# Performance work log

Hardware: AMD Instinct MI355X
Metric: run time of the kernel (lower is better)

The kernel has to match this reference:

```python
import jax, jax.numpy as jnp
import numpy as np

F = 50  # number of feature fields

def setup_inputs() -> dict:
    key = jax.random.key(0)
    k1, k2, k3, k4 = jax.random.split(key, 4)
    B, D, A = 4096, 16, 32
    return {
        "feat_emb": jax.random.normal(k1, (B, F, D), dtype=jnp.float32),
        "W": jax.random.normal(k2, (D, A), dtype=jnp.float32) * 0.1,
        "h": jax.random.normal(k3, (A,), dtype=jnp.float32),
        "p_vec": jax.random.normal(k4, (D,), dtype=jnp.float32),
    }

def reference(feat_emb, W, h, p_vec):
    # build_cross: upper-triangular field pairs (i < j)
    row, col = np.triu_indices(F, k=1)              # each [P], P = F*(F-1)/2
    p = feat_emb[:, row]                             # [B, P, D]
    q = feat_emb[:, col]                             # [B, P, D]
    inter = p * q                                    # pairwise interaction [B, P, D]
    # AttLayer: Dense(no bias) -> relu -> contract with h -> softmax over pairs
    att_signal = jax.nn.relu(jnp.einsum('bpd,da->bpa', inter, W))  # [B, P, A]
    scores = jnp.einsum('bpa,a->bp', att_signal, h)                # [B, P]
    att = jax.nn.softmax(scores, axis=1)                           # [B, P]
    # attention-weighted sum-pooling over pairs
    pooled = jnp.einsum('bp,bpd->bd', att, inter)                  # [B, D]
    # dropout omitted (inference); final projection and reduce
    out = jnp.einsum('bd,d->b', pooled, p_vec)[:, None]            # [B, 1]
    return out
```

## Files before the change

### kernel.cpp

```cpp
#include <hip/hip_runtime.h>
#include <math.h>


#define FF 50
#define DD 16
#define AA 32
#define NP 1225
#define NT 39
#define NTP 40
#define ERS 24
#define EBS (FF * ERS)
#define BPB 8
#define NTHR 512
#define SGN (NT * 32)

typedef _Float16 half8 __attribute__((ext_vector_type(8)));
typedef _Float16 half4 __attribute__((ext_vector_type(4)));
typedef _Float16 half2v __attribute__((ext_vector_type(2)));
typedef __fp16   fh2    __attribute__((ext_vector_type(2)));
typedef float    floatx16 __attribute__((ext_vector_type(16)));

__global__ __launch_bounds__(NTHR, 2) void afm_kernel(
    const float* __restrict__ feat,
    const float* __restrict__ W,
    const float* __restrict__ h,
    const float* __restrict__ pvec,
    float* __restrict__ out,
    int Btot)
{
  __shared__ __align__(16) _Float16 eh[BPB * EBS];
  __shared__ unsigned int tbl[NTP * 32];
  __shared__ __align__(16) float2 sg[BPB * SGN];

  const int tid    = threadIdx.x;
  const int lane   = tid & 63;
  const int wave   = tid >> 6;
  const int halfid = lane >> 5;
  const int n      = lane & 31;
  const int b0     = blockIdx.x * BPB;

  for (int s = tid; s < BPB * 200; s += NTHR) {
    int bl  = s / 200;
    int rem = s - bl * 200;
    int bb  = b0 + bl;
    if (bb < Btot) {
      float4 v4 = ((const float4*)feat)[(size_t)bb * 200 + rem];
      half4 hv;
      hv[0] = (_Float16)v4.x; hv[1] = (_Float16)v4.y;
      hv[2] = (_Float16)v4.z; hv[3] = (_Float16)v4.w;
      int row = rem >> 2, q = rem & 3;
      *(half4*)(&eh[bl * EBS + row * ERS + q * 4]) = hv;
    }
  }

  for (int q = tid; q < NTP * 32; q += NTHR) {
    int t = ((q >> 6) << 1) | (q & 1);
    int nn = (q >> 1) & 31;
    int p = t * 32 + nn;
    unsigned ent = 0;
    if (p < NP) {
      int rad = 9801 - 8 * p;
      int i = (int)((99.0f - sqrtf((float)rad)) * 0.5f);
      if (i < 0) i = 0; if (i > 48) i = 48;
      int off = (i * (99 - i)) >> 1;
      if (off > p) { --i; off = (i * (99 - i)) >> 1; }
      else {
        int off1 = ((i + 1) * (98 - i)) >> 1;
        if (off1 <= p) { ++i; off = off1; }
      }
      int j = p - off + i + 1;
      ent = ((unsigned)(i * 48) << 16) | (unsigned)(j * 48);
    }
    tbl[q] = ent;
  }

  const float LOG2E = 1.4426950408889634f;
  half8 A0;
  #pragma unroll
  for (int jj = 0; jj < 8; ++jj)
    A0[jj] = (_Float16)W[(halfid * 8 + jj) * AA + n];
  float hreg[16];
  #pragma unroll
  for (int r = 0; r < 16; ++r)
    hreg[r] = h[(r & 3) + 8 * (r >> 2) + 4 * halfid] * LOG2E;
  fh2 pv2[4];
  #pragma unroll
  for (int q = 0; q < 4; ++q) {
    pv2[q][0] = (__fp16)pvec[halfid * 8 + 2 * q];
    pv2[q][1] = (__fp16)pvec[halfid * 8 + 2 * q + 1];
  }
  const floatx16 ZACC = (floatx16)0.0f;

  __syncthreads();

  const char* eb = (const char*)(eh + wave * EBS) + halfid * 16;
  float2* sgw = sg + wave * SGN;
  const unsigned int* tpair = tbl + 2 * n;

  auto core = [&](unsigned oi, unsigned oj, float& vout, float& gout) {
    half8 Bi = *(const half8*)(eb + oi);
    half8 Bj = *(const half8*)(eb + oj);
    half8 Bv = Bi * Bj;
    floatx16 z = __builtin_amdgcn_mfma_f32_32x32x16_f16(A0, Bv, ZACC, 0, 0, 0);
    float a0 = 0.f, a1 = 0.f, a2 = 0.f, a3 = 0.f;
    #pragma unroll
    for (int r = 0; r < 16; r += 4) {
      a0 = fmaf(fmaxf(z[r + 0], 0.f), hreg[r + 0], a0);
      a1 = fmaf(fmaxf(z[r + 1], 0.f), hreg[r + 1], a1);
      a2 = fmaf(fmaxf(z[r + 2], 0.f), hreg[r + 2], a2);
      a3 = fmaf(fmaxf(z[r + 3], 0.f), hreg[r + 3], a3);
    }
    float v = (a0 + a1) + (a2 + a3);
#if __has_builtin(__builtin_amdgcn_fdot2)
    fh2 q0 = __builtin_bit_cast(fh2, (half2v)__builtin_shufflevector(Bv, Bv, 0, 1));
    fh2 q1 = __builtin_bit_cast(fh2, (half2v)__builtin_shufflevector(Bv, Bv, 2, 3));
    fh2 q2 = __builtin_bit_cast(fh2, (half2v)__builtin_shufflevector(Bv, Bv, 4, 5));
    fh2 q3 = __builtin_bit_cast(fh2, (half2v)__builtin_shufflevector(Bv, Bv, 6, 7));
    float g = __builtin_amdgcn_fdot2(q1, pv2[1],
              __builtin_amdgcn_fdot2(q0, pv2[0], 0.f, false), false)
            + __builtin_amdgcn_fdot2(q3, pv2[3],
              __builtin_amdgcn_fdot2(q2, pv2[2], 0.f, false), false);
#else
    float g = 0.f;
    #pragma unroll
    for (int k = 0; k < 8; ++k)
      g = fmaf((float)Bv[k], (float)((const __fp16*)pv2)[k], g);
#endif
    vout = v + __shfl_xor(v, 32, 64);
    gout = g + __shfl_xor(g, 32, 64);
  };

  for (int th = 0; th < 19; ++th) {
    uint2 ij2 = *(const uint2*)(tpair + th * 64);
    float v0, g0, v1, g1;
    core(ij2.x >> 16, ij2.x & 0xffffu, v0, g0);
    core(ij2.y >> 16, ij2.y & 0xffffu, v1, g1);
    if (lane < 32) {
      sgw[(2 * th)     * 32 + n] = make_float2(v0, g0);
      sgw[(2 * th + 1) * 32 + n] = make_float2(v1, g1);
    }
  }
  {
    unsigned ij = tpair[19 * 64];
    float v, g;
    core(ij >> 16, ij & 0xffffu, v, g);
    if (n >= 9) v = -3.0e38f;
    if (lane < 32) sgw[38 * 32 + n] = make_float2(v, g);
  }

  float den = 0.f, num = 0.f;
  for (int p = lane; p < SGN; p += 64) {
    float2 s2 = sgw[p];
    float e = exp2f(s2.x);
    den += e;
    num = fmaf(e, s2.y, num);
  }
  #pragma unroll
  for (int mask = 32; mask >= 1; mask >>= 1) {
    den += __shfl_xor(den, mask, 64);
    num += __shfl_xor(num, mask, 64);
  }
  const int b = b0 + wave;
  if (lane == 0 && b < Btot) out[b] = num / den;
}

extern "C" void kernel_launch(void* const* d_in, const int* in_sizes, int n_in,
                              void* d_out, int out_size, void* d_ws, size_t ws_size,
                              hipStream_t stream) {
  const float* feat = (const float*)d_in[0];
  const float* W    = (const float*)d_in[1];
  const float* h    = (const float*)d_in[2];
  const float* pvec = (const float*)d_in[3];
  float* out = (float*)d_out;
  const int B = in_sizes[0] / (FF * DD);
  afm_kernel<<<(B + BPB - 1) / BPB, NTHR, 0, stream>>>(feat, W, h, pvec, out, B);
}
```

Before: 96.25 us.

## Fuse softmax accumulation into the pair loop and drop the LDS score buffer

Exponentiation and the numerator/denominator accumulation now happen in registers right after each MFMA tile, instead of staging scores and projections in an 80KB shared buffer and making a second pass over it. The cross-half shuffle for the projection term is removed. Each half-wave therefore adds the exponential once, which doubles the denominator, and the final divide multiplies the numerator by 2 to compensate. With the shared memory freed, blocks shrink to 4 batch rows and 256 threads, and the occupancy hint rises from 2 to 4 so more blocks fit per CU. The hardware exp2 builtin replaces exp2f. As before, no max is subtracted, so the computation still relies on scores staying in range.

```diff
diff --git a/kernel.cpp b/kernel.cpp
--- a/kernel.cpp
+++ b/kernel.cpp
@@ -10,9 +10,8 @@
 #define NTP 40
 #define ERS 24
 #define EBS (FF * ERS)
-#define BPB 8
-#define NTHR 512
-#define SGN (NT * 32)
+#define BPB 4
+#define NTHR 256
 
 typedef _Float16 half8 __attribute__((ext_vector_type(8)));
 typedef _Float16 half4 __attribute__((ext_vector_type(4)));
@@ -20,7 +19,7 @@
 typedef __fp16   fh2    __attribute__((ext_vector_type(2)));
 typedef float    floatx16 __attribute__((ext_vector_type(16)));
 
-__global__ __launch_bounds__(NTHR, 2) void afm_kernel(
+__global__ __launch_bounds__(NTHR, 4) void afm_kernel(
     const float* __restrict__ feat,
     const float* __restrict__ W,
     const float* __restrict__ h,
@@ -30,7 +29,6 @@
 {
   __shared__ __align__(16) _Float16 eh[BPB * EBS];
   __shared__ unsigned int tbl[NTP * 32];
-  __shared__ __align__(16) float2 sg[BPB * SGN];
 
   const int tid    = threadIdx.x;
   const int lane   = tid & 63;
@@ -94,7 +92,6 @@
   __syncthreads();
 
   const char* eb = (const char*)(eh + wave * EBS) + halfid * 16;
-  float2* sgw = sg + wave * SGN;
   const unsigned int* tpair = tbl + 2 * n;
 
   auto core = [&](unsigned oi, unsigned oj, float& vout, float& gout) {
@@ -111,57 +108,55 @@
       a3 = fmaf(fmaxf(z[r + 3], 0.f), hreg[r + 3], a3);
     }
     float v = (a0 + a1) + (a2 + a3);
+    vout = v + __shfl_xor(v, 32, 64);
 #if __has_builtin(__builtin_amdgcn_fdot2)
     fh2 q0 = __builtin_bit_cast(fh2, (half2v)__builtin_shufflevector(Bv, Bv, 0, 1));
     fh2 q1 = __builtin_bit_cast(fh2, (half2v)__builtin_shufflevector(Bv, Bv, 2, 3));
     fh2 q2 = __builtin_bit_cast(fh2, (half2v)__builtin_shufflevector(Bv, Bv, 4, 5));
     fh2 q3 = __builtin_bit_cast(fh2, (half2v)__builtin_shufflevector(Bv, Bv, 6, 7));
-    float g = __builtin_amdgcn_fdot2(q1, pv2[1],
-              __builtin_amdgcn_fdot2(q0, pv2[0], 0.f, false), false)
-            + __builtin_amdgcn_fdot2(q3, pv2[3],
-              __builtin_amdgcn_fdot2(q2, pv2[2], 0.f, false), false);
+    gout = __builtin_amdgcn_fdot2(q1, pv2[1],
+           __builtin_amdgcn_fdot2(q0, pv2[0], 0.f, false), false)
+         + __builtin_amdgcn_fdot2(q3, pv2[3],
+           __builtin_amdgcn_fdot2(q2, pv2[2], 0.f, false), false);
 #else
-    float g = 0.f;
+    float gp = 0.f;
     #pragma unroll
     for (int k = 0; k < 8; ++k)
-      g = fmaf((float)Bv[k], (float)((const __fp16*)pv2)[k], g);
+      gp = fmaf((float)Bv[k], (float)((const __fp16*)pv2)[k], gp);
+    gout = gp;
 #endif
-    vout = v + __shfl_xor(v, 32, 64);
-    gout = g + __shfl_xor(g, 32, 64);
   };
 
+#if __has_builtin(__builtin_amdgcn_exp2f)
+  #define EXP2(x) __builtin_amdgcn_exp2f(x)
+#else
+  #define EXP2(x) exp2f(x)
+#endif
+
+  float den = 0.f, num = 0.f;
   for (int th = 0; th < 19; ++th) {
     uint2 ij2 = *(const uint2*)(tpair + th * 64);
-    float v0, g0, v1, g1;
-    core(ij2.x >> 16, ij2.x & 0xffffu, v0, g0);
-    core(ij2.y >> 16, ij2.y & 0xffffu, v1, g1);
-    if (lane < 32) {
-      sgw[(2 * th)     * 32 + n] = make_float2(v0, g0);
-      sgw[(2 * th + 1) * 32 + n] = make_float2(v1, g1);
-    }
+    float v, g;
+    core(ij2.x >> 16, ij2.x & 0xffffu, v, g);
+    { float e = EXP2(v); den += e; num = fmaf(e, g, num); }
+    core(ij2.y >> 16, ij2.y & 0xffffu, v, g);
+    { float e = EXP2(v); den += e; num = fmaf(e, g, num); }
   }
   {
     unsigned ij = tpair[19 * 64];
     float v, g;
     core(ij >> 16, ij & 0xffffu, v, g);
     if (n >= 9) v = -3.0e38f;
-    if (lane < 32) sgw[38 * 32 + n] = make_float2(v, g);
+    float e = EXP2(v); den += e; num = fmaf(e, g, num);
   }
 
-  float den = 0.f, num = 0.f;
-  for (int p = lane; p < SGN; p += 64) {
-    float2 s2 = sgw[p];
-    float e = exp2f(s2.x);
-    den += e;
-    num = fmaf(e, s2.y, num);
-  }
   #pragma unroll
   for (int mask = 32; mask >= 1; mask >>= 1) {
     den += __shfl_xor(den, mask, 64);
     num += __shfl_xor(num, mask, 64);
   }
   const int b = b0 + wave;
-  if (lane == 0 && b < Btot) out[b] = num / den;
+  if (lane == 0 && b < Btot) out[b] = (2.0f * num) / den;
 }
 
 extern "C" void kernel_launch(void* const* d_in, const int* in_sizes, int n_in,
```

After: 86.02 us. 10.6% less time.
